# Kernel optimization log

Measured on AMD Instinct MI355X. Metric: run time of the kernel, lower is better.

## Reference

```python
import jax, jax.numpy as jnp
import numpy as np

DIM = 1024
HEADS = 16
DIM_HEAD = 64
INNER = HEADS * DIM_HEAD
EPS_NORM = 1e-12  # F.normalize eps
LN_EPS = 1e-5     # torch F.layer_norm default eps


def setup_inputs() -> dict:
    key = jax.random.key(0)
    ks = jax.random.split(key, 6)
    x = jax.random.normal(ks[0], (8, 1024, DIM), dtype=jnp.float32)
    ln_gamma = jnp.ones((DIM,), jnp.float32)
    q_gamma = jnp.ones((HEADS, 1, DIM_HEAD), jnp.float32)
    k_gamma = jnp.ones((HEADS, 1, DIM_HEAD), jnp.float32)
    # nn.Linear default init ~ U(-1/sqrt(fan_in), 1/sqrt(fan_in))
    w_qkv = jax.random.uniform(ks[1], (DIM, 3 * INNER), jnp.float32, -1.0, 1.0) / np.sqrt(DIM)
    w_out = jax.random.uniform(ks[2], (INNER, DIM), jnp.float32, -1.0, 1.0) / np.sqrt(INNER)
    return {"x": x, "ln_gamma": ln_gamma, "q_gamma": q_gamma, "k_gamma": k_gamma,
            "w_qkv": w_qkv, "w_out": w_out}


def _layer_norm(x, gamma):
    mu = jnp.mean(x, axis=-1, keepdims=True)
    var = jnp.var(x, axis=-1, keepdims=True)
    return (x - mu) * jax.lax.rsqrt(var + LN_EPS) * gamma  # beta is zeros buffer


def _rms(x, gamma):
    # F.normalize(x, dim=-1) * sqrt(d) * gamma
    n = jnp.linalg.norm(x, axis=-1, keepdims=True)
    normed = x / jnp.maximum(n, EPS_NORM)
    return normed * (DIM_HEAD ** 0.5) * gamma


def reference(x, ln_gamma, q_gamma, k_gamma, w_qkv, w_out):
    b, n, _ = x.shape
    h, d = HEADS, DIM_HEAD
    xn = _layer_norm(x, ln_gamma)
    qkv = xn @ w_qkv  # [b, n, 3*inner]
    q, k, v = jnp.split(qkv, 3, axis=-1)
    # b n (h d) -> b h n d
    to_heads = lambda t: t.reshape(b, n, h, d).transpose(0, 2, 1, 3)
    q, k, v = to_heads(q), to_heads(k), to_heads(v)
    q = _rms(q, q_gamma)
    k = _rms(k, k_gamma)
    dots = jnp.einsum('bhid,bhjd->bhij', q, k)  # no extra scale (scale baked into RMSNorm)
    attn = jax.nn.softmax(dots, axis=-1)
    out = jnp.einsum('bhij,bhjd->bhid', attn, v)
    out = out.transpose(0, 2, 1, 3).reshape(b, n, h * d)
    return out @ w_out
```

## Files before the change

### kernel.cpp

```cpp
#include <hip/hip_runtime.h>
#include <hip/hip_bf16.h>
#include <math.h>

#define DIMX   1024
#define HEADS  16
#define DH     64
#define NB     8
#define NSEQ   1024
#define ROWS   (NB * NSEQ)
#define QKVW   (3 * DIMX)
#define LOG2E  1.44269504088896f

typedef _Float16 half8 __attribute__((ext_vector_type(8)));
typedef _Float16 half4 __attribute__((ext_vector_type(4)));
typedef float floatx4 __attribute__((ext_vector_type(4)));

#define GLD_LDS16(gptr, lptr) __builtin_amdgcn_global_load_lds( \
    (const __attribute__((address_space(1))) void*)(gptr),      \
    (__attribute__((address_space(3))) void*)(lptr), 16, 0, 0)

__device__ __forceinline__ float fexp2(float x) {
#if __has_builtin(__builtin_amdgcn_exp2f)
    return __builtin_amdgcn_exp2f(x);
#else
    return __expf(x * 0.69314718056f);
#endif
}

__global__ __launch_bounds__(256) void lnw_kernel(const float* __restrict__ x,
                                                  const float* __restrict__ gamma,
                                                  const float* __restrict__ Wq,
                                                  const float* __restrict__ Wo,
                                                  _Float16* __restrict__ xn,
                                                  _Float16* __restrict__ WqT,
                                                  _Float16* __restrict__ WoT) {
    __shared__ float tile[32][33];
    __shared__ float sbuf[4], ssbuf[4];
    int t = threadIdx.x;

    if (blockIdx.x < ROWS) {
        int row = blockIdx.x;
        const float* xr = x + (size_t)row * DIMX;
        _Float16* xo = xn + (size_t)row * DIMX;

        float4 v = ((const float4*)xr)[t];
        float s  = v.x + v.y + v.z + v.w;
        float ss = v.x*v.x + v.y*v.y + v.z*v.z + v.w*v.w;
        #pragma unroll
        for (int o = 32; o > 0; o >>= 1) {
            s  += __shfl_down(s, o);
            ss += __shfl_down(ss, o);
        }
        int lane = t & 63, wid = t >> 6;
        if (lane == 0) { sbuf[wid] = s; ssbuf[wid] = ss; }
        __syncthreads();
        if (t == 0) {
            float a = 0.f, b2 = 0.f;
            for (int i = 0; i < 4; i++) { a += sbuf[i]; b2 += ssbuf[i]; }
            sbuf[0] = a; ssbuf[0] = b2;
        }
        __syncthreads();
        float mean = sbuf[0] * (1.0f / DIMX);
        float var  = ssbuf[0] * (1.0f / DIMX) - mean * mean;
        float rstd = rsqrtf(var + 1e-5f);

        float4 g = ((const float4*)gamma)[t];
        half4 o;
        o.x = (_Float16)((v.x - mean) * rstd * g.x);
        o.y = (_Float16)((v.y - mean) * rstd * g.y);
        o.z = (_Float16)((v.z - mean) * rstd * g.z);
        o.w = (_Float16)((v.w - mean) * rstd * g.w);
        *(half4*)(xo + t * 4) = o;
    } else {
        int idx = blockIdx.x - ROWS;
        int bx = idx & 127, by = idx >> 7;
        const float* W; _Float16* WT; int N, n0;
        if (bx < 96) { W = Wq; WT = WqT; N = QKVW; n0 = bx * 32; }
        else         { W = Wo; WT = WoT; N = DIMX; n0 = (bx - 96) * 32; }
        int k0 = by * 32;
        int tx = t & 31, ty = t >> 5;
        #pragma unroll
        for (int i = 0; i < 32; i += 8)
            tile[ty + i][tx] = W[(size_t)(k0 + ty + i) * N + n0 + tx];
        __syncthreads();
        #pragma unroll
        for (int i = 0; i < 32; i += 8)
            WT[(size_t)(n0 + ty + i) * 1024 + k0 + tx] = (_Float16)tile[tx][ty + i];
    }
}

__global__ __launch_bounds__(512, 2) void hgemm_qkv_big(const _Float16* __restrict__ A,
                                                        const _Float16* __restrict__ BT,
                                                        const float* __restrict__ qg,
                                                        const float* __restrict__ kg,
                                                        _Float16* __restrict__ qf,
                                                        _Float16* __restrict__ kf,
                                                        _Float16* __restrict__ vt) {
    extern __shared__ char smem[];
    const int K = DIMX;

    int t = threadIdx.x;
    int wave = t >> 6, lane = t & 63;
    int quad = lane >> 4, l16 = lane & 15;
    int wm = (wave >> 1) * 64;
    int wn = (wave & 1) * 64;
    size_t m0 = (size_t)blockIdx.y * 256, n0 = (size_t)blockIdx.x * 128;

    floatx4 acc[4][4] = {};

    int lr = lane >> 2;
    int ksw = (lane & 3) ^ ((lane >> 3) & 3);
    const _Float16* ag = A  + (m0 + wave * 32 + lr) * (size_t)K + ksw * 8;
    const _Float16* bg = BT + (n0 + wave * 16 + lr) * (size_t)K + ksw * 8;
    int rsw = (l16 >> 1) & 3;

#define STAGE(s) do { int _sb = (int)(s) & 3; size_t _ko = (size_t)(s) * 32;    \
        char* _bb = smem + _sb * 24576;                                         \
        GLD_LDS16(ag + _ko,          _bb + wave * 2048);                        \
        GLD_LDS16(ag + 16 * K + _ko, _bb + wave * 2048 + 1024);                 \
        GLD_LDS16(bg + _ko,          _bb + 16384 + wave * 1024);                \
    } while (0)

#define STEP_BODY(s, STAGE_STMT, WAIT_STMT) do {                                \
        int _rb = (int)(s) & 3;                                                 \
        const _Float16* As_ = (const _Float16*)(smem + _rb * 24576);            \
        const _Float16* Bs_ = (const _Float16*)(smem + _rb * 24576 + 16384);    \
        STAGE_STMT;                                                             \
        half8 af[4], bf[4];                                                     \
        _Pragma("unroll")                                                       \
        for (int mf = 0; mf < 4; mf++)                                          \
            af[mf] = *(const half8*)&As_[(wm + mf * 16 + l16) * 32              \
                                         + (quad ^ rsw) * 8];                   \
        _Pragma("unroll")                                                       \
        for (int nf = 0; nf < 4; nf++)                                          \
            bf[nf] = *(const half8*)&Bs_[(wn + nf * 16 + l16) * 32              \
                                         + (quad ^ rsw) * 8];                   \
        __builtin_amdgcn_s_setprio(1);                                          \
        _Pragma("unroll")                                                       \
        for (int mf = 0; mf < 4; mf++)                                          \
            _Pragma("unroll")                                                   \
            for (int nf = 0; nf < 4; nf++)                                      \
                acc[mf][nf] = __builtin_amdgcn_mfma_f32_16x16x32_f16(           \
                    bf[nf], af[mf], acc[mf][nf], 0, 0, 0);                      \
        __builtin_amdgcn_s_setprio(0);                                          \
        WAIT_STMT;                                                              \
        __builtin_amdgcn_s_barrier();                                           \
        asm volatile("" ::: "memory");                                          \
    } while (0)

    STAGE(0); STAGE(1); STAGE(2);
    asm volatile("s_waitcnt vmcnt(6)" ::: "memory");
    __builtin_amdgcn_s_barrier();
    asm volatile("" ::: "memory");

    for (int s = 0; s < 29; s++)
        STEP_BODY(s, STAGE(s + 3),
                  asm volatile("s_waitcnt vmcnt(6)" ::: "memory"));
    STEP_BODY(29, ((void)0), asm volatile("s_waitcnt vmcnt(3)" ::: "memory"));
    STEP_BODY(30, ((void)0), asm volatile("s_waitcnt vmcnt(0)" ::: "memory"));
    STEP_BODY(31, ((void)0), ((void)0));

#undef STAGE
#undef STEP_BODY

    int which = (int)(n0 >> 10);
    int nloc  = ((int)n0 & 1023) + wn;
    int h = nloc >> 6;

    if (which < 2) {
        const float* g = (which == 0) ? qg : kg;
        float emul = (which == 0) ? LOG2E : 1.0f;
        _Float16* dstbuf = (which == 0) ? qf : kf;
        #pragma unroll
        for (int mf = 0; mf < 4; mf++) {
            size_t tok = m0 + wm + mf * 16 + l16;
            int b = (int)(tok >> 10), ntk = (int)(tok & 1023);
            _Float16* dst = dstbuf + (((size_t)(b * 16 + h)) * 1024 + ntk) * 64;
            float ss = 0.f;
            #pragma unroll
            for (int nf = 0; nf < 4; nf++)
                #pragma unroll
                for (int r = 0; r < 4; r++) ss += acc[mf][nf][r] * acc[mf][nf][r];
            ss += __shfl_xor(ss, 16);
            ss += __shfl_xor(ss, 32);
            float scale = 8.0f * emul / fmaxf(sqrtf(ss), 1e-12f);
            #pragma unroll
            for (int nf = 0; nf < 4; nf++) {
                half4 p;
                #pragma unroll
                for (int r = 0; r < 4; r++)
                    p[r] = (_Float16)(acc[mf][nf][r] * scale *
                                      g[h * 64 + nf * 16 + quad * 4 + r]);
                *(half4*)(dst + nf * 16 + quad * 4) = p;
            }
        }
    } else {
        #pragma unroll
        for (int mf = 0; mf < 4; mf++) {
            size_t tok = m0 + wm + mf * 16 + l16;
            int b = (int)(tok >> 10), ntk = (int)(tok & 1023);
            int nt = ntk >> 6;
            _Float16* vd = vt + ((size_t)((b * 16 + h) * 16 + nt) * 64) * 64
                              + mf * 16 + l16;
            #pragma unroll
            for (int nf = 0; nf < 4; nf++)
                #pragma unroll
                for (int r = 0; r < 4; r++)
                    vd[(size_t)(nf * 16 + quad * 4 + r) * 64] =
                        (_Float16)acc[mf][nf][r];
        }
    }
}

__global__ __launch_bounds__(256) void hgemm_qkv_small(const _Float16* __restrict__ A,
                                                       const _Float16* __restrict__ BT,
                                                       const float* __restrict__ qg,
                                                       const float* __restrict__ kg,
                                                       _Float16* __restrict__ qf,
                                                       _Float16* __restrict__ kf,
                                                       _Float16* __restrict__ vt) {
    __shared__ _Float16 As[128 * 64];
    __shared__ _Float16 Bs[128 * 64];
    const int K = DIMX;

    int t = threadIdx.x;
    int wave = t >> 6, lane = t & 63;
    int quad = lane >> 4, l16 = lane & 15;
    int wm = (wave >> 1) * 64;
    int wn = (wave & 1) * 64;
    size_t m0 = (size_t)blockIdx.y * 128, n0 = (size_t)blockIdx.x * 128;

    floatx4 acc[4][4] = {};

    int sr = t >> 3, sg = t & 7;
    int swz = sg ^ (sr & 7);
    const _Float16* ag = A  + (m0 + sr) * (size_t)K + swz * 8;
    const _Float16* bg = BT + (n0 + sr) * (size_t)K + swz * 8;
    char* lA = (char*)As + wave * 1024;
    char* lB = (char*)Bs + wave * 1024;

    for (int k0 = 0; k0 < K; k0 += 64) {
        #pragma unroll
        for (int i = 0; i < 4; i++) {
            GLD_LDS16(ag + (size_t)(i * 32) * K + k0, lA + i * 4096);
            GLD_LDS16(bg + (size_t)(i * 32) * K + k0, lB + i * 4096);
        }
        __syncthreads();

        half8 af[2][4], bf[2][4];
        #pragma unroll
        for (int kk = 0; kk < 2; kk++) {
            #pragma unroll
            for (int mf = 0; mf < 4; mf++)
                af[kk][mf] = *(const half8*)&As[(wm + mf * 16 + l16) * 64
                                 + (((kk * 4 + quad) ^ (l16 & 7)) * 8)];
            #pragma unroll
            for (int nf = 0; nf < 4; nf++)
                bf[kk][nf] = *(const half8*)&Bs[(wn + nf * 16 + l16) * 64
                                 + (((kk * 4 + quad) ^ (l16 & 7)) * 8)];
        }

        #pragma unroll
        for (int kk = 0; kk < 2; kk++)
            #pragma unroll
            for (int mf = 0; mf < 4; mf++)
                #pragma unroll
                for (int nf = 0; nf < 4; nf++)
                    acc[mf][nf] = __builtin_amdgcn_mfma_f32_16x16x32_f16(
                        bf[kk][nf], af[kk][mf], acc[mf][nf], 0, 0, 0);
        __syncthreads();
    }

    int which = (int)(n0 >> 10);
    int nloc  = ((int)n0 & 1023) + wn;
    int h = nloc >> 6;

    if (which < 2) {
        const float* g = (which == 0) ? qg : kg;
        float emul = (which == 0) ? LOG2E : 1.0f;
        _Float16* dstbuf = (which == 0) ? qf : kf;
        #pragma unroll
        for (int mf = 0; mf < 4; mf++) {
            size_t tok = m0 + wm + mf * 16 + l16;
            int b = (int)(tok >> 10), ntk = (int)(tok & 1023);
            _Float16* dst = dstbuf + (((size_t)(b * 16 + h)) * 1024 + ntk) * 64;
            float ss = 0.f;
            #pragma unroll
            for (int nf = 0; nf < 4; nf++)
                #pragma unroll
                for (int r = 0; r < 4; r++) ss += acc[mf][nf][r] * acc[mf][nf][r];
            ss += __shfl_xor(ss, 16);
            ss += __shfl_xor(ss, 32);
            float scale = 8.0f * emul / fmaxf(sqrtf(ss), 1e-12f);
            #pragma unroll
            for (int nf = 0; nf < 4; nf++) {
                half4 p;
                #pragma unroll
                for (int r = 0; r < 4; r++)
                    p[r] = (_Float16)(acc[mf][nf][r] * scale *
                                      g[h * 64 + nf * 16 + quad * 4 + r]);
                *(half4*)(dst + nf * 16 + quad * 4) = p;
            }
        }
    } else {
        #pragma unroll
        for (int mf = 0; mf < 4; mf++) {
            size_t tok = m0 + wm + mf * 16 + l16;
            int b = (int)(tok >> 10), ntk = (int)(tok & 1023);
            int nt = ntk >> 6;
            _Float16* vd = vt + ((size_t)((b * 16 + h) * 16 + nt) * 64) * 64
                              + mf * 16 + l16;
            #pragma unroll
            for (int nf = 0; nf < 4; nf++)
                #pragma unroll
                for (int r = 0; r < 4; r++)
                    vd[(size_t)(nf * 16 + quad * 4 + r) * 64] =
                        (_Float16)acc[mf][nf][r];
        }
    }
}

__global__ __launch_bounds__(256, 3) void flash_kernel(const _Float16* __restrict__ qf,
                                                       const _Float16* __restrict__ kf,
                                                       const _Float16* __restrict__ vt,
                                                       _Float16* __restrict__ obuf) {
    __shared__ _Float16 Ks[2][64 * 64];
    __shared__ _Float16 VTs[2][64 * 64];
    __shared__ _Float16 Ps[4][16][68];

    int t = threadIdx.x;
    int wave = t >> 6, lane = t & 63;
    int quad = lane >> 4, l16 = lane & 15;
    int bh = blockIdx.x & 127, qt = blockIdx.x >> 7;

    const _Float16* qb = qf + ((size_t)bh * 1024 + qt * 128) * 64;
    const _Float16* kb = kf + (size_t)bh * 65536;
    const _Float16* vb = vt + (size_t)bh * 65536;

    half8 aq[2][2];
    #pragma unroll
    for (int st = 0; st < 2; st++) {
        const _Float16* qrow = qb + (wave * 32 + st * 16 + l16) * 64;
        aq[st][0] = *(const half8*)(qrow + quad * 8);
        aq[st][1] = *(const half8*)(qrow + 32 + quad * 8);
    }

    floatx4 o[2][4] = {};
    float m_i[2] = {-INFINITY, -INFINITY};
    float l_i[2] = {0.f, 0.f};

    int sr = t >> 3;
    int sg = t & 7;
    int swz = sg ^ (sr & 7);

    #pragma unroll
    for (int i = 0; i < 2; i++) {
        GLD_LDS16(kb + (i * 32 + sr) * 64 + swz * 8, (char*)Ks[0]  + wave * 1024 + i * 4096);
        GLD_LDS16(vb + (i * 32 + sr) * 64 + swz * 8, (char*)VTs[0] + wave * 1024 + i * 4096);
    }

    for (int kt = 0; kt < 16; kt++) {
        int cur = kt & 1;
        __syncthreads();

        if (kt < 15) {
            const _Float16* kn = kb + (size_t)(kt + 1) * 4096;
            const _Float16* vn = vb + (size_t)(kt + 1) * 4096;
            #pragma unroll
            for (int i = 0; i < 2; i++) {
                GLD_LDS16(kn + (i * 32 + sr) * 64 + swz * 8,
                          (char*)Ks[cur ^ 1]  + wave * 1024 + i * 4096);
                GLD_LDS16(vn + (i * 32 + sr) * 64 + swz * 8,
                          (char*)VTs[cur ^ 1] + wave * 1024 + i * 4096);
            }
        }

        #pragma unroll
        for (int st = 0; st < 2; st++) {
            floatx4 sc[4] = {};
            #pragma unroll
            for (int kc = 0; kc < 2; kc++) {
                #pragma unroll
                for (int nf = 0; nf < 4; nf++) {
                    half8 ak = *(const half8*)&Ks[cur][(nf * 16 + l16) * 64
                                    + (((kc * 4 + quad) ^ (l16 & 7)) * 8)];
                    sc[nf] = __builtin_amdgcn_mfma_f32_16x16x32_f16(
                        ak, aq[st][kc], sc[nf], 0, 0, 0);
                }
            }

            float mx = sc[0][0];
            #pragma unroll
            for (int nf = 0; nf < 4; nf++)
                #pragma unroll
                for (int r = 0; r < 4; r++) mx = fmaxf(mx, sc[nf][r]);
            mx = fmaxf(mx, __shfl_xor(mx, 16));
            mx = fmaxf(mx, __shfl_xor(mx, 32));
            if (mx > m_i[st]) {
                float alpha = fexp2(m_i[st] - mx);
                l_i[st] *= alpha;
                #pragma unroll
                for (int nf = 0; nf < 4; nf++) o[st][nf] *= alpha;
                m_i[st] = mx;
            }
            float mcur = m_i[st];
            float psum = 0.f;
            #pragma unroll
            for (int nf = 0; nf < 4; nf++)
                #pragma unroll
                for (int r = 0; r < 4; r++) {
                    float p = fexp2(sc[nf][r] - mcur);
                    sc[nf][r] = p;
                    psum += p;
                }
            l_i[st] += psum;

            #pragma unroll
            for (int nf = 0; nf < 4; nf++) {
                half4 p4;
                #pragma unroll
                for (int r = 0; r < 4; r++) p4[r] = (_Float16)sc[nf][r];
                *(half4*)&Ps[wave][l16][nf * 16 + quad * 4] = p4;
            }

            #pragma unroll
            for (int kc = 0; kc < 2; kc++) {
                half4 p0 = *(const half4*)&Ps[wave][l16][kc * 32 + quad * 8];
                half4 p1 = *(const half4*)&Ps[wave][l16][kc * 32 + quad * 8 + 4];
                half8 bp;
                #pragma unroll
                for (int j = 0; j < 4; j++) { bp[j] = p0[j]; bp[4 + j] = p1[j]; }
                #pragma unroll
                for (int nf = 0; nf < 4; nf++) {
                    half8 av = *(const half8*)&VTs[cur][(nf * 16 + l16) * 64
                                    + (((kc * 4 + quad) ^ (l16 & 7)) * 8)];
                    o[st][nf] = __builtin_amdgcn_mfma_f32_16x16x32_f16(
                        av, bp, o[st][nf], 0, 0, 0);
                }
            }
        }
    }

    int b = bh >> 4, h = bh & 15;
    #pragma unroll
    for (int st = 0; st < 2; st++) {
        float lsum = l_i[st];
        lsum += __shfl_xor(lsum, 16);
        lsum += __shfl_xor(lsum, 32);
        float inv = 1.0f / lsum;
        size_t row = (size_t)b * NSEQ + qt * 128 + wave * 32 + st * 16 + l16;
        #pragma unroll
        for (int nf = 0; nf < 4; nf++) {
            half4 o4;
            #pragma unroll
            for (int r = 0; r < 4; r++) o4[r] = (_Float16)(o[st][nf][r] * inv);
            *(half4*)(obuf + row * 1024 + h * 64 + nf * 16 + quad * 4) = o4;
        }
    }
}

__global__ __launch_bounds__(256) void hgemm_out(const _Float16* __restrict__ A,
                                                 const _Float16* __restrict__ BT,
                                                 float* __restrict__ C) {
    __shared__ _Float16 As[128 * 64];
    __shared__ _Float16 Bs[128 * 64];
    const int K = DIMX, N = DIMX;

    int t = threadIdx.x;
    int wave = t >> 6, lane = t & 63;
    int quad = lane >> 4, l16 = lane & 15;
    int wm = (wave >> 1) * 64, wn = (wave & 1) * 64;
    size_t m0 = (size_t)blockIdx.y * 128, n0 = (size_t)blockIdx.x * 128;

    floatx4 acc[4][4] = {};

    int sr = t >> 3, sg = t & 7;
    int swz = sg ^ (sr & 7);
    const _Float16* ag = A  + (m0 + sr) * (size_t)K + swz * 8;
    const _Float16* bg = BT + (n0 + sr) * (size_t)K + swz * 8;
    char* lA = (char*)As + wave * 1024;
    char* lB = (char*)Bs + wave * 1024;

    for (int k0 = 0; k0 < K; k0 += 64) {
        #pragma unroll
        for (int i = 0; i < 4; i++) {
            GLD_LDS16(ag + (size_t)(i * 32) * K + k0, lA + i * 4096);
            GLD_LDS16(bg + (size_t)(i * 32) * K + k0, lB + i * 4096);
        }
        __syncthreads();

        half8 af[2][4], bf[2][4];
        #pragma unroll
        for (int kk = 0; kk < 2; kk++) {
            #pragma unroll
            for (int mf = 0; mf < 4; mf++)
                af[kk][mf] = *(const half8*)&As[(wm + mf * 16 + l16) * 64
                                 + (((kk * 4 + quad) ^ (l16 & 7)) * 8)];
            #pragma unroll
            for (int nf = 0; nf < 4; nf++)
                bf[kk][nf] = *(const half8*)&Bs[(wn + nf * 16 + l16) * 64
                                 + (((kk * 4 + quad) ^ (l16 & 7)) * 8)];
        }

        #pragma unroll
        for (int kk = 0; kk < 2; kk++)
            #pragma unroll
            for (int mf = 0; mf < 4; mf++)
                #pragma unroll
                for (int nf = 0; nf < 4; nf++)
                    acc[mf][nf] = __builtin_amdgcn_mfma_f32_16x16x32_f16(
                        bf[kk][nf], af[kk][mf], acc[mf][nf], 0, 0, 0);
        __syncthreads();
    }

    #pragma unroll
    for (int mf = 0; mf < 4; mf++) {
        size_t tok = m0 + wm + mf * 16 + l16;
        #pragma unroll
        for (int nf = 0; nf < 4; nf++)
            *(floatx4*)(C + tok * N + n0 + wn + nf * 16 + quad * 4) = acc[mf][nf];
    }
}

extern "C" void kernel_launch(void* const* d_in, const int* in_sizes, int n_in,
                              void* d_out, int out_size, void* d_ws, size_t ws_size,
                              hipStream_t stream) {
    const float* x     = (const float*)d_in[0];
    const float* ln_g  = (const float*)d_in[1];
    const float* q_g   = (const float*)d_in[2];
    const float* k_g   = (const float*)d_in[3];
    const float* w_qkv = (const float*)d_in[4];
    const float* w_out = (const float*)d_in[5];
    float* out = (float*)d_out;

    char* base = (char*)d_ws;
    _Float16* xn    = (_Float16*)(base);
    _Float16* wqkvT = (_Float16*)(base + (16ull << 20));
    _Float16* woutT = (_Float16*)(base + (22ull << 20));
    _Float16* qf    = (_Float16*)(base + (24ull << 20));
    _Float16* kf    = (_Float16*)(base + (40ull << 20));
    _Float16* vt    = (_Float16*)(base + (56ull << 20));
    _Float16* obuf  = (_Float16*)(base + (72ull << 20));

    static int use_big = -1;
    if (use_big < 0) {
        int ok = 0;
        if (hipFuncSetAttribute((const void*)hgemm_qkv_big,
                                hipFuncAttributeMaxDynamicSharedMemorySize,
                                98304) == hipSuccess) {
            hipFuncAttributes fa;
            if (hipFuncGetAttributes(&fa, (const void*)hgemm_qkv_big) == hipSuccess
                && fa.maxDynamicSharedSizeBytes >= 98304)
                ok = 1;
        }
        use_big = ok;
    }

    lnw_kernel<<<ROWS + 4096, 256, 0, stream>>>(x, ln_g, w_qkv, w_out,
                                                xn, wqkvT, woutT);

    if (use_big) {
        dim3 g1(QKVW / 128, ROWS / 256);
        hgemm_qkv_big<<<g1, 512, 98304, stream>>>(xn, wqkvT, q_g, k_g, qf, kf, vt);
    } else {
        dim3 g1(QKVW / 128, ROWS / 128);
        hgemm_qkv_small<<<g1, 256, 0, stream>>>(xn, wqkvT, q_g, k_g, qf, kf, vt);
    }

    flash_kernel<<<NB * HEADS * (NSEQ / 128), 256, 0, stream>>>(qf, kf, vt, obuf);

    dim3 g2(DIMX / 128, ROWS / 128);
    hgemm_out<<<g2, 256, 0, stream>>>(obuf, woutT, out);
}
```

Measured before the change: 265.6 us.

## Enlarge QKV GEMM tile to 256x256 with 3-stage split A/B staging and block swizzle

The QKV GEMM block tile grows from 256x128 to 256x256, so each wave now computes a 128x64 sub-tile with 8x4 accumulators. The pipeline changes from a 4-buffer, depth-3 prefetch to a 3-buffer, depth-2 scheme, and the A and B global-to-LDS loads are interleaved between the two MFMA halves. Block IDs are remapped so neighbouring blocks share input tiles in L2. The aim is more operand reuse per LDS byte and better cache locality, at the cost of more registers, a shallower prefetch and fewer blocks (384 instead of 768).

```diff
diff --git a/kernel.cpp b/kernel.cpp
--- a/kernel.cpp
+++ b/kernel.cpp
@@ -97,74 +97,100 @@
                                                         _Float16* __restrict__ kf,
                                                         _Float16* __restrict__ vt) {
     extern __shared__ char smem[];
+    _Float16* smemh = (_Float16*)smem;
     const int K = DIMX;
 
     int t = threadIdx.x;
     int wave = t >> 6, lane = t & 63;
     int quad = lane >> 4, l16 = lane & 15;
-    int wm = (wave >> 1) * 64;
-    int wn = (wave & 1) * 64;
-    size_t m0 = (size_t)blockIdx.y * 256, n0 = (size_t)blockIdx.x * 128;
-
-    floatx4 acc[4][4] = {};
-
-    int lr = lane >> 2;
-    int ksw = (lane & 3) ^ ((lane >> 3) & 3);
-    const _Float16* ag = A  + (m0 + wave * 32 + lr) * (size_t)K + ksw * 8;
-    const _Float16* bg = BT + (n0 + wave * 16 + lr) * (size_t)K + ksw * 8;
+    int mw = wave >> 2;
+    int nw = wave & 3;
+
+    int id  = blockIdx.y * 12 + blockIdx.x;
+    int swz_id = (id & 7) * 48 + (id >> 3);
+    int bx = swz_id % 12, by = swz_id / 12;
+    size_t m0 = (size_t)by * 256, n0 = (size_t)bx * 256;
+
+    floatx4 acc[8][4] = {};
+
+    int srow   = lane >> 2;
+    int schunk = (lane & 3) ^ ((lane >> 3) & 3);
+    const _Float16* agA = A  + (m0 + wave * 32 + srow) * (size_t)K + schunk * 8;
+    const _Float16* bgB = BT + (n0 + wave * 32 + srow) * (size_t)K + schunk * 8;
     int rsw = (l16 >> 1) & 3;
 
-#define STAGE(s) do { int _sb = (int)(s) & 3; size_t _ko = (size_t)(s) * 32;    \
-        char* _bb = smem + _sb * 24576;                                         \
-        GLD_LDS16(ag + _ko,          _bb + wave * 2048);                        \
-        GLD_LDS16(ag + 16 * K + _ko, _bb + wave * 2048 + 1024);                 \
-        GLD_LDS16(bg + _ko,          _bb + 16384 + wave * 1024);                \
+#define STAGE_A(TT, SB) do {                                                    \
+        char* d_ = smem + (SB) * 32768 + wave * 2048;                           \
+        const _Float16* g_ = agA + (size_t)(TT) * 32;                           \
+        GLD_LDS16(g_, d_);                                                      \
+        GLD_LDS16(g_ + 16 * (size_t)K, d_ + 1024);                              \
     } while (0)
 
-#define STEP_BODY(s, STAGE_STMT, WAIT_STMT) do {                                \
-        int _rb = (int)(s) & 3;                                                 \
-        const _Float16* As_ = (const _Float16*)(smem + _rb * 24576);            \
-        const _Float16* Bs_ = (const _Float16*)(smem + _rb * 24576 + 16384);    \
-        STAGE_STMT;                                                             \
+#define STAGE_B(TT, SB) do {                                                    \
+        char* d_ = smem + (SB) * 32768 + 16384 + wave * 2048;                   \
+        const _Float16* g_ = bgB + (size_t)(TT) * 32;                           \
+        GLD_LDS16(g_, d_);                                                      \
+        GLD_LDS16(g_ + 16 * (size_t)K, d_ + 1024);                              \
+    } while (0)
+
+#define TILE(ST, RB, SB, DOST, WAIT_STMT) do {                                  \
+        const _Float16* As_ = smemh + (RB) * 16384;                             \
+        const _Float16* Bs_ = As_ + 8192;                                       \
         half8 af[4], bf[4];                                                     \
         _Pragma("unroll")                                                       \
-        for (int mf = 0; mf < 4; mf++)                                          \
-            af[mf] = *(const half8*)&As_[(wm + mf * 16 + l16) * 32              \
-                                         + (quad ^ rsw) * 8];                   \
+        for (int i = 0; i < 4; i++)                                             \
+            af[i] = *(const half8*)&As_[(mw * 128 + i * 16 + l16) * 32          \
+                                        + (quad ^ rsw) * 8];                    \
         _Pragma("unroll")                                                       \
         for (int nf = 0; nf < 4; nf++)                                          \
-            bf[nf] = *(const half8*)&Bs_[(wn + nf * 16 + l16) * 32              \
+            bf[nf] = *(const half8*)&Bs_[(nw * 64 + nf * 16 + l16) * 32         \
                                          + (quad ^ rsw) * 8];                   \
+        if (DOST) STAGE_A(ST, SB);                                              \
         __builtin_amdgcn_s_setprio(1);                                          \
         _Pragma("unroll")                                                       \
-        for (int mf = 0; mf < 4; mf++)                                          \
+        for (int i = 0; i < 4; i++)                                             \
             _Pragma("unroll")                                                   \
             for (int nf = 0; nf < 4; nf++)                                      \
-                acc[mf][nf] = __builtin_amdgcn_mfma_f32_16x16x32_f16(           \
-                    bf[nf], af[mf], acc[mf][nf], 0, 0, 0);                      \
+                acc[i][nf] = __builtin_amdgcn_mfma_f32_16x16x32_f16(            \
+                    bf[nf], af[i], acc[i][nf], 0, 0, 0);                        \
+        __builtin_amdgcn_s_setprio(0);                                          \
+        _Pragma("unroll")                                                       \
+        for (int i = 0; i < 4; i++)                                             \
+            af[i] = *(const half8*)&As_[(mw * 128 + (4 + i) * 16 + l16) * 32    \
+                                        + (quad ^ rsw) * 8];                    \
+        if (DOST) STAGE_B(ST, SB);                                              \
+        __builtin_amdgcn_s_setprio(1);                                          \
+        _Pragma("unroll")                                                       \
+        for (int i = 0; i < 4; i++)                                             \
+            _Pragma("unroll")                                                   \
+            for (int nf = 0; nf < 4; nf++)                                      \
+                acc[4 + i][nf] = __builtin_amdgcn_mfma_f32_16x16x32_f16(        \
+                    bf[nf], af[i], acc[4 + i][nf], 0, 0, 0);                    \
         __builtin_amdgcn_s_setprio(0);                                          \
         WAIT_STMT;                                                              \
         __builtin_amdgcn_s_barrier();                                           \
         asm volatile("" ::: "memory");                                          \
     } while (0)
 
-    STAGE(0); STAGE(1); STAGE(2);
-    asm volatile("s_waitcnt vmcnt(6)" ::: "memory");
+    STAGE_A(0, 0); STAGE_B(0, 0); STAGE_A(1, 1); STAGE_B(1, 1);
+    asm volatile("s_waitcnt vmcnt(4)" ::: "memory");
     __builtin_amdgcn_s_barrier();
     asm volatile("" ::: "memory");
 
-    for (int s = 0; s < 29; s++)
-        STEP_BODY(s, STAGE(s + 3),
-                  asm volatile("s_waitcnt vmcnt(6)" ::: "memory"));
-    STEP_BODY(29, ((void)0), asm volatile("s_waitcnt vmcnt(3)" ::: "memory"));
-    STEP_BODY(30, ((void)0), asm volatile("s_waitcnt vmcnt(0)" ::: "memory"));
-    STEP_BODY(31, ((void)0), ((void)0));
-
-#undef STAGE
-#undef STEP_BODY
+    for (int T = 0; T < 30; T += 3) {
+        TILE(T + 2, 0, 2, 1, asm volatile("s_waitcnt vmcnt(4)" ::: "memory"));
+        TILE(T + 3, 1, 0, 1, asm volatile("s_waitcnt vmcnt(4)" ::: "memory"));
+        TILE(T + 4, 2, 1, 1, asm volatile("s_waitcnt vmcnt(4)" ::: "memory"));
+    }
+    TILE(0, 0, 0, 0, asm volatile("s_waitcnt vmcnt(0)" ::: "memory"));
+    TILE(0, 1, 0, 0, ((void)0));
+
+#undef TILE
+#undef STAGE_A
+#undef STAGE_B
 
     int which = (int)(n0 >> 10);
-    int nloc  = ((int)n0 & 1023) + wn;
+    int nloc  = ((int)n0 & 1023) + nw * 64;
     int h = nloc >> 6;
 
     if (which < 2) {
@@ -172,8 +198,8 @@
         float emul = (which == 0) ? LOG2E : 1.0f;
         _Float16* dstbuf = (which == 0) ? qf : kf;
         #pragma unroll
-        for (int mf = 0; mf < 4; mf++) {
-            size_t tok = m0 + wm + mf * 16 + l16;
+        for (int mf = 0; mf < 8; mf++) {
+            size_t tok = m0 + mw * 128 + mf * 16 + l16;
             int b = (int)(tok >> 10), ntk = (int)(tok & 1023);
             _Float16* dst = dstbuf + (((size_t)(b * 16 + h)) * 1024 + ntk) * 64;
             float ss = 0.f;
@@ -196,12 +222,12 @@
         }
     } else {
         #pragma unroll
-        for (int mf = 0; mf < 4; mf++) {
-            size_t tok = m0 + wm + mf * 16 + l16;
+        for (int mf = 0; mf < 8; mf++) {
+            size_t tok = m0 + mw * 128 + mf * 16 + l16;
             int b = (int)(tok >> 10), ntk = (int)(tok & 1023);
             int nt = ntk >> 6;
             _Float16* vd = vt + ((size_t)((b * 16 + h) * 16 + nt) * 64) * 64
-                              + mf * 16 + l16;
+                              + (mf & 3) * 16 + l16;
             #pragma unroll
             for (int nf = 0; nf < 4; nf++)
                 #pragma unroll
@@ -560,7 +586,7 @@
                                                 xn, wqkvT, woutT);
 
     if (use_big) {
-        dim3 g1(QKVW / 128, ROWS / 256);
+        dim3 g1(QKVW / 256, ROWS / 256);
         hgemm_qkv_big<<<g1, 512, 98304, stream>>>(xn, wqkvT, q_g, k_g, qf, kf, vt);
     } else {
         dim3 g1(QKVW / 128, ROWS / 128);
```

New measurement: 263.7 us. Within noise of the previous version (-0.7%).
